# Kernel tuning notes

Measured on AMD Instinct MI355X. Metric: run time of the kernel, lower is better.

The kernel has to match this reference:

```python
import jax, jax.numpy as jnp
import numpy as np

B, S, N_USERS, N_ITEMS, E = 32, 512, 10000, 10000, 128


def setup_inputs() -> dict:
    key = jax.random.key(0)
    ks = jax.random.split(key, 8)
    users = jax.random.randint(ks[0], (B, S), 0, N_USERS, dtype=jnp.int32)
    items = jax.random.randint(ks[1], (B, S), 0, N_ITEMS, dtype=jnp.int32)
    user_mem0 = jax.random.normal(ks[2], (B, N_USERS, E), dtype=jnp.float32)
    item_mem0 = jax.random.normal(ks[3], (B, N_ITEMS, E), dtype=jnp.float32)
    # GRUCell(2E, E): w_ih (3E, 2E), w_hh (3E, E)
    w_ih = jax.random.normal(ks[4], (3 * E, 2 * E), dtype=jnp.float32) * 0.05
    w_hh = jax.random.normal(ks[5], (3 * E, E), dtype=jnp.float32) * 0.05
    b_ih = jax.random.normal(ks[6], (3 * E,), dtype=jnp.float32) * 0.05
    b_hh = jax.random.normal(ks[7], (3 * E,), dtype=jnp.float32) * 0.05
    return {"users": users, "items": items, "user_mem0": user_mem0,
            "item_mem0": item_mem0, "w_ih": w_ih, "w_hh": w_hh,
            "b_ih": b_ih, "b_hh": b_hh}


def _gru_cell(x, h, w_ih, w_hh, b_ih, b_hh):
    # torch.nn.GRUCell semantics
    gi = x @ w_ih.T + b_ih  # (B, 3E)
    gh = h @ w_hh.T + b_hh  # (B, 3E)
    i_r, i_z, i_n = jnp.split(gi, 3, axis=-1)
    h_r, h_z, h_n = jnp.split(gh, 3, axis=-1)
    r = jax.nn.sigmoid(i_r + h_r)
    z = jax.nn.sigmoid(i_z + h_z)
    n = jnp.tanh(i_n + r * h_n)
    return (1.0 - z) * n + z * h


def reference(users, items, user_mem0, item_mem0, w_ih, w_hh, b_ih, b_hh):
    batch = jnp.arange(users.shape[0])

    def step(carry, uv):
        um, im = carry
        u, it = uv  # (B,), (B,)
        ue = um[batch, u]   # gather (B, E)
        ie = im[batch, it]  # gather (B, E)
        xu = jnp.concatenate([ue, ie], axis=-1)
        xi = jnp.concatenate([ie, ue], axis=-1)
        nu = _gru_cell(xu, ue, w_ih, w_hh, b_ih, b_hh)
        ni = _gru_cell(xi, ie, w_ih, w_hh, b_ih, b_hh)
        um = um.at[batch, u].set(nu)   # scatter write
        im = im.at[batch, it].set(ni)  # scatter write
        return (um, im), (nu, ni)

    (_, _), (u_out, i_out) = jax.lax.scan(
        step, (user_mem0, item_mem0), (users.T, items.T))
    # (S, B, E) -> (B, S, E)
    return jnp.transpose(u_out, (1, 0, 2)), jnp.transpose(i_out, (1, 0, 2))
```

## Files before the change

kernel.cpp:

```cpp
#include <hip/hip_runtime.h>

#define NB 32
#define NS 512
#define NE 128
#define NU 10000

#define WS_PREVU 0
#define WS_PREVI 16384
#define WS_CNT0  32768
#define WS_CNT1  32769
#define WS_LCNT  32770
#define WS_G0    32832
#define WS_G1    49216
#define WS_LATE  65600
#define WS_WBF   81984

typedef __attribute__((ext_vector_type(8))) short bf16x8;
typedef __attribute__((ext_vector_type(4))) float f32x4;

__device__ __forceinline__ unsigned short f2bf(float f) {
    unsigned int u = __float_as_uint(f);
    u += 0x7fff + ((u >> 16) & 1);
    return (unsigned short)(u >> 16);
}

__global__ __launch_bounds__(512) void prep1_kernel(
    const int* __restrict__ users, const int* __restrict__ items,
    const float* __restrict__ w_ih, const float* __restrict__ w_hh, int* ws)
{
    const int blk = blockIdx.x, tid = threadIdx.x;
    if (blk >= 64) {
        const int base = (blk - 64) * 4096 + tid * 8;
        const int r = base >> 7, k = base & 127;
        const float* src;
        if (r < 384)      src = w_ih + (size_t)r * 256 + k;
        else if (r < 768) src = w_ih + (size_t)(r - 384) * 256 + 128 + k;
        else              src = w_hh + (size_t)(r - 768) * 128 + k;
        unsigned short* wbf = (unsigned short*)(ws + WS_WBF);
#pragma unroll
        for (int j = 0; j < 8; ++j) wbf[base + j] = f2bf(src[j]);
        return;
    }
    const int b = blk >> 1, which = blk & 1;
    if (blk == 0 && tid < 2) ws[WS_CNT0 + tid] = 0;
    __shared__ int s[NS];
    s[tid] = (which ? items : users)[b * NS + tid];
    __syncthreads();
    const int mid = s[tid];
    int p = -1;
    for (int u = tid - 1; u >= 0 && p < 0; u -= 8) {
        int vals[8];
#pragma unroll
        for (int j = 0; j < 8; ++j) {
            const int uu = u - j;
            vals[j] = (uu >= 0) ? s[uu] : -1;
        }
#pragma unroll
        for (int j = 0; j < 8; ++j)
            if (p < 0 && vals[j] == mid) p = u - j;
    }
    ws[(which ? WS_PREVI : WS_PREVU) + b * NS + tid] = p;
}

__global__ __launch_bounds__(512) void prep2_kernel(int* ws)
{
    const int b = blockIdx.x, tid = threadIdx.x;
    __shared__ short s_pU[NS], s_pI[NS];
    __shared__ unsigned char s_r[NS];
    __shared__ int c0, c1, base0, base1, s_chg;
    const int pU = ws[WS_PREVU + (b << 9) + tid];
    const int pI = ws[WS_PREVI + (b << 9) + tid];
    s_pU[tid] = (short)pU;
    s_pI[tid] = (short)pI;
    s_r[tid] = (pU < 0 && pI < 0) ? 0 : 255;
    if (tid == 0) { c0 = 0; c1 = 0; }
    __syncthreads();
    for (int pass = 0; pass < 16; ++pass) {
        if (tid == 0) s_chg = 0;
        __syncthreads();
        if (s_r[tid] == 255) {
            const int ru = pU < 0 ? -1 : (int)s_r[pU];
            const int ri = pI < 0 ? -1 : (int)s_r[pI];
            if (ru != 255 && ri != 255) {
                int rr = 1 + (ru > ri ? ru : ri);
                if (rr > 2) rr = 2;
                s_r[tid] = (unsigned char)rr;
                s_chg = 1;
            }
        }
        __syncthreads();
        if (!s_chg) break;
    }
    const int r = s_r[tid];
    int slot = -1;
    if (r == 0)      slot = atomicAdd(&c0, 1);
    else if (r == 1) slot = atomicAdd(&c1, 1);
    __syncthreads();
    if (tid == 0) {
        base0 = atomicAdd(&ws[WS_CNT0], c0);
        base1 = atomicAdd(&ws[WS_CNT1], c1);
    }
    __syncthreads();
    const int node = (b << 9) + tid;
    if (r == 0)      ws[WS_G0 + base0 + slot] = node;
    else if (r == 1) ws[WS_G1 + base1 + slot] = node;
    if (tid == 0) {
        int n = 0;
        for (int t = 0; t < NS; ++t)
            if (s_r[t] >= 2) { ws[WS_LATE + (b << 9) + n] = t; ++n; }
        ws[WS_LCNT + b] = n;
    }
}

__global__ __launch_bounds__(512, 1) void round_gemm(
    const int* __restrict__ users, const int* __restrict__ items,
    const float* __restrict__ umem0, const float* __restrict__ imem0,
    const float* __restrict__ b_ih, const float* __restrict__ b_hh,
    const int* __restrict__ ws, float* uout, float* iout,
    int cnt_off, int list_off)
{
    const int count = ws[cnt_off];
    const int nch = (count + 7) >> 3;
    if ((int)blockIdx.x >= nch) return;
    const int tid = threadIdx.x;
    const int lane = tid & 63, wave = tid >> 6;
    const int col = lane & 15, kgrp = lane >> 4;

    __shared__ __align__(16) float yl[16 * 1156];
    __shared__ __align__(16) float xf[16 * 132];
    __shared__ __align__(16) unsigned short xb[16 * 136];
    __shared__ float b6[768];
    __shared__ unsigned long long srcs[16];
    __shared__ unsigned long long hdst[16];

    for (int i = tid; i < 768; i += 512)
        b6[i] = i < 384 ? b_ih[i] : b_hh[i - 384];

    const unsigned short* wbf = (const unsigned short*)(ws + WS_WBF);
    bf16x8 wfrag[9][4];
#pragma unroll
    for (int m9 = 0; m9 < 9; ++m9) {
        const int row = wave * 144 + m9 * 16 + col;
#pragma unroll
        for (int kt = 0; kt < 4; ++kt)
            wfrag[m9][kt] = *(const bf16x8*)&wbf[row * 128 + kt * 32 + kgrp * 8];
    }

    const int* glist = ws + list_off;
    const int* prevU = ws + WS_PREVU;
    const int* prevI = ws + WS_PREVI;

    for (int ch = blockIdx.x; ch < nch; ch += gridDim.x) {
        if (tid < 16) {
            const int j = ch * 8 + (tid >> 1);
            unsigned long long sp = 0, hd = 0;
            if (j < count) {
                const int node = glist[j];
                const int bb = node >> 9;
                const int cell = tid & 1;
                const int p = cell ? prevI[node] : prevU[node];
                const float* s;
                if (p < 0) {
                    const int ix = cell ? items[node] : users[node];
                    s = (cell ? imem0 : umem0) + ((size_t)bb * NU + ix) * NE;
                } else {
                    s = (cell ? iout : uout) + ((size_t)((bb << 9) + p)) * NE;
                }
                sp = (unsigned long long)s;
                hd = (unsigned long long)((cell ? iout : uout) + (size_t)node * NE);
            }
            srcs[tid] = sp; hdst[tid] = hd;
        }
        __syncthreads();
        {
            const int c = tid >> 5, e4 = (tid & 31) * 4;
            const float* s = (const float*)srcs[c];
            if (s) {
                const float4 v = *(const float4*)(s + e4);
                *(float4*)&xf[c * 132 + e4] = v;
                ushort4 w4;
                w4.x = f2bf(v.x); w4.y = f2bf(v.y);
                w4.z = f2bf(v.z); w4.w = f2bf(v.w);
                *(ushort4*)&xb[c * 136 + e4] = w4;
            }
        }
        __syncthreads();
        {
            bf16x8 bfrag[4];
#pragma unroll
            for (int kt = 0; kt < 4; ++kt)
                bfrag[kt] = *(const bf16x8*)&xb[col * 136 + kt * 32 + kgrp * 8];
            f32x4 acc[9];
#pragma unroll
            for (int m9 = 0; m9 < 9; ++m9) acc[m9] = (f32x4){0.f, 0.f, 0.f, 0.f};
#pragma unroll
            for (int kt = 0; kt < 4; ++kt)
#pragma unroll
                for (int m9 = 0; m9 < 9; ++m9)
                    acc[m9] = __builtin_amdgcn_mfma_f32_16x16x32_bf16(
                        wfrag[m9][kt], bfrag[kt], acc[m9], 0, 0, 0);
#pragma unroll
            for (int m9 = 0; m9 < 9; ++m9)
                *(f32x4*)&yl[col * 1156 + wave * 144 + m9 * 16 + kgrp * 4] = acc[m9];
        }
        __syncthreads();
#pragma unroll
        for (int it = 0; it < 4; ++it) {
            const int idx = tid + it * 512;
            const int c = idx >> 7, e = idx & 127;
            float* hb = (float*)hdst[c];
            if (hb) {
                const float* ys = &yl[c * 1156];
                const float* yo = &yl[(c ^ 1) * 1156];
                const float gir = ys[e]        + yo[384 + e] + b6[e];
                const float giz = ys[128 + e]  + yo[512 + e] + b6[128 + e];
                const float gin = ys[256 + e]  + yo[640 + e] + b6[256 + e];
                const float ghr = ys[768 + e]  + b6[384 + e];
                const float ghz = ys[896 + e]  + b6[512 + e];
                const float ghn = ys[1024 + e] + b6[640 + e];
                const float rr = 1.f / (1.f + __expf(-(gir + ghr)));
                const float z  = 1.f / (1.f + __expf(-(giz + ghz)));
                const float pre = gin + rr * ghn;
                const float n = 2.f / (1.f + __expf(-2.f * pre)) - 1.f;
                hb[e] = (1.f - z) * n + z * xf[c * 132 + e];
            }
        }
        __syncthreads();
    }
}

__global__ __launch_bounds__(512, 1) void cleanup_kernel(
    const int* __restrict__ users, const int* __restrict__ items,
    const float* __restrict__ umem0, const float* __restrict__ imem0,
    const float* __restrict__ b_ih, const float* __restrict__ b_hh,
    const int* __restrict__ ws, float* uout, float* iout)
{
    const int b = blockIdx.x;
    const int n = ws[WS_LCNT + b];
    if (n == 0) return;
    const int tid = threadIdx.x;
    const int lane = tid & 63, wave = tid >> 6;
    const int col = lane & 15, kgrp = lane >> 4;

    __shared__ __align__(16) float yl[2][1156];
    __shared__ __align__(16) float xf[2][132];
    __shared__ __align__(16) unsigned short xb[2][136];
    __shared__ float b6[768];
    __shared__ const float* srcs[2];

    for (int i = tid; i < 768; i += 512)
        b6[i] = i < 384 ? b_ih[i] : b_hh[i - 384];

    const unsigned short* wbf = (const unsigned short*)(ws + WS_WBF);
    bf16x8 wfrag[9][4];
#pragma unroll
    for (int m9 = 0; m9 < 9; ++m9) {
        const int row = wave * 144 + m9 * 16 + col;
#pragma unroll
        for (int kt = 0; kt < 4; ++kt)
            wfrag[m9][kt] = *(const bf16x8*)&wbf[row * 128 + kt * 32 + kgrp * 8];
    }

    const int* prevU = ws + WS_PREVU;
    const int* prevI = ws + WS_PREVI;

    for (int k = 0; k < n; ++k) {
        const int t = ws[WS_LATE + (b << 9) + k];
        const int node = (b << 9) + t;
        if (tid < 2) {
            const int cell = tid;
            const int p = cell ? prevI[node] : prevU[node];
            const float* sp;
            if (p < 0) {
                const int ix = cell ? items[node] : users[node];
                sp = (cell ? imem0 : umem0) + ((size_t)b * NU + ix) * NE;
            } else {
                sp = (cell ? iout : uout) + ((size_t)((b << 9) + p)) * NE;
            }
            srcs[cell] = sp;
        }
        __syncthreads();
        if (tid < 64) {
            const int c = tid >> 5, e4 = (tid & 31) * 4;
            const float4 v = *(const float4*)(srcs[c] + e4);
            *(float4*)&xf[c][e4] = v;
            ushort4 w4;
            w4.x = f2bf(v.x); w4.y = f2bf(v.y);
            w4.z = f2bf(v.z); w4.w = f2bf(v.w);
            *(ushort4*)&xb[c][e4] = w4;
        }
        __syncthreads();
        {
            const int bc = col & 1;
            bf16x8 bfrag[4];
#pragma unroll
            for (int kt = 0; kt < 4; ++kt)
                bfrag[kt] = *(const bf16x8*)&xb[bc][kt * 32 + kgrp * 8];
            f32x4 acc[9];
#pragma unroll
            for (int m9 = 0; m9 < 9; ++m9) acc[m9] = (f32x4){0.f, 0.f, 0.f, 0.f};
#pragma unroll
            for (int kt = 0; kt < 4; ++kt)
#pragma unroll
                for (int m9 = 0; m9 < 9; ++m9)
                    acc[m9] = __builtin_amdgcn_mfma_f32_16x16x32_bf16(
                        wfrag[m9][kt], bfrag[kt], acc[m9], 0, 0, 0);
            if (col < 2) {
#pragma unroll
                for (int m9 = 0; m9 < 9; ++m9)
                    *(f32x4*)&yl[col][wave * 144 + m9 * 16 + kgrp * 4] = acc[m9];
            }
        }
        __syncthreads();
        if (tid < 256) {
            const int c = tid >> 7, e = tid & 127;
            const float* ys = yl[c];
            const float* yo = yl[c ^ 1];
            const float gir = ys[e]        + yo[384 + e] + b6[e];
            const float giz = ys[128 + e]  + yo[512 + e] + b6[128 + e];
            const float gin = ys[256 + e]  + yo[640 + e] + b6[256 + e];
            const float ghr = ys[768 + e]  + b6[384 + e];
            const float ghz = ys[896 + e]  + b6[512 + e];
            const float ghn = ys[1024 + e] + b6[640 + e];
            const float rr = 1.f / (1.f + __expf(-(gir + ghr)));
            const float z  = 1.f / (1.f + __expf(-(giz + ghz)));
            const float pre = gin + rr * ghn;
            const float nn = 2.f / (1.f + __expf(-2.f * pre) ) - 1.f;
            (c ? iout : uout)[(size_t)node * NE + e] =
                (1.f - z) * nn + z * xf[c][e];
        }
        __threadfence();
        __syncthreads();
    }
}

extern "C" void kernel_launch(void* const* d_in, const int* in_sizes, int n_in,
                              void* d_out, int out_size, void* d_ws, size_t ws_size,
                              hipStream_t stream) {
    const int*   users = (const int*)d_in[0];
    const int*   items = (const int*)d_in[1];
    const float* umem0 = (const float*)d_in[2];
    const float* imem0 = (const float*)d_in[3];
    const float* w_ih  = (const float*)d_in[4];
    const float* w_hh  = (const float*)d_in[5];
    const float* b_ih  = (const float*)d_in[6];
    const float* b_hh  = (const float*)d_in[7];

    float* uout = (float*)d_out;
    float* iout = uout + (size_t)NB * NS * NE;
    int* ws = (int*)d_ws;

    prep1_kernel<<<100, 512, 0, stream>>>(users, items, w_ih, w_hh, ws);
    prep2_kernel<<<NB, 512, 0, stream>>>(ws);
    round_gemm<<<256, 512, 0, stream>>>(users, items, umem0, imem0,
                                        b_ih, b_hh, ws, uout, iout,
                                        WS_CNT0, WS_G0);
    round_gemm<<<256, 512, 0, stream>>>(users, items, umem0, imem0,
                                        b_ih, b_hh, ws, uout, iout,
                                        WS_CNT1, WS_G1);
    cleanup_kernel<<<NB, 512, 0, stream>>>(users, items, umem0, imem0,
                                           b_ih, b_hh, ws, uout, iout);
}
```

Measured before the change: 122.5 us.

## Fuse prep kernels, add third dependency round, prefetch per-batch chunk gathers

Merges the two prep kernels into one per-batch kernel that finds previous occurrences and assigns dependency levels, now capping at level 3 so a third batched GEMM round runs before the serial cleanup. Round lists become per-batch, without global atomics, and each block handles up to 8 chunks of one batch. It gathers all chunk inputs up front into registers to hide memory latency. Lighter barriers replace __syncthreads. This shrinks the serial tail work and removes one launch, at the cost of an extra round launch and more register pressure.

```diff
diff --git a/kernel.cpp b/kernel.cpp
--- a/kernel.cpp
+++ b/kernel.cpp
@@ -7,13 +7,11 @@
 
 #define WS_PREVU 0
 #define WS_PREVI 16384
-#define WS_CNT0  32768
-#define WS_CNT1  32769
-#define WS_LCNT  32770
-#define WS_G0    32832
-#define WS_G1    49216
-#define WS_LATE  65600
-#define WS_WBF   81984
+#define WS_RCNT  32768
+#define WS_LCNT  32864
+#define WS_GL    32896
+#define WS_LATE  82048
+#define WS_WBF   98432
 
 typedef __attribute__((ext_vector_type(8))) short bf16x8;
 typedef __attribute__((ext_vector_type(4))) float f32x4;
@@ -24,13 +22,19 @@
     return (unsigned short)(u >> 16);
 }
 
-__global__ __launch_bounds__(512) void prep1_kernel(
+#define BARRIER() do { \
+    asm volatile("s_waitcnt lgkmcnt(0)" ::: "memory"); \
+    __builtin_amdgcn_s_barrier(); \
+    __builtin_amdgcn_sched_barrier(0); \
+} while (0)
+
+__global__ __launch_bounds__(512) void prep_kernel(
     const int* __restrict__ users, const int* __restrict__ items,
     const float* __restrict__ w_ih, const float* __restrict__ w_hh, int* ws)
 {
     const int blk = blockIdx.x, tid = threadIdx.x;
-    if (blk >= 64) {
-        const int base = (blk - 64) * 4096 + tid * 8;
+    if (blk >= 32) {
+        const int base = (blk - 32) * 4096 + tid * 8;
         const int r = base >> 7, k = base & 127;
         const float* src;
         if (r < 384)      src = w_ih + (size_t)r * 256 + k;
@@ -41,49 +45,51 @@
         for (int j = 0; j < 8; ++j) wbf[base + j] = f2bf(src[j]);
         return;
     }
-    const int b = blk >> 1, which = blk & 1;
-    if (blk == 0 && tid < 2) ws[WS_CNT0 + tid] = 0;
-    __shared__ int s[NS];
-    s[tid] = (which ? items : users)[b * NS + tid];
+    const int b = blk;
+    __shared__ int s_u[NS], s_i[NS];
+    __shared__ unsigned char s_r[NS];
+    __shared__ int cnt[3], s_chg;
+    s_u[tid] = users[b * NS + tid];
+    s_i[tid] = items[b * NS + tid];
+    if (tid < 3) cnt[tid] = 0;
     __syncthreads();
-    const int mid = s[tid];
-    int p = -1;
-    for (int u = tid - 1; u >= 0 && p < 0; u -= 8) {
+    const int mu = s_u[tid], mi = s_i[tid];
+    int pu = -1, pi = -1;
+    for (int u = tid - 1; u >= 0 && pu < 0; u -= 8) {
         int vals[8];
 #pragma unroll
         for (int j = 0; j < 8; ++j) {
             const int uu = u - j;
-            vals[j] = (uu >= 0) ? s[uu] : -1;
+            vals[j] = (uu >= 0) ? s_u[uu] : -1;
         }
 #pragma unroll
         for (int j = 0; j < 8; ++j)
-            if (p < 0 && vals[j] == mid) p = u - j;
-    }
-    ws[(which ? WS_PREVI : WS_PREVU) + b * NS + tid] = p;
-}
-
-__global__ __launch_bounds__(512) void prep2_kernel(int* ws)
-{
-    const int b = blockIdx.x, tid = threadIdx.x;
-    __shared__ short s_pU[NS], s_pI[NS];
-    __shared__ unsigned char s_r[NS];
-    __shared__ int c0, c1, base0, base1, s_chg;
-    const int pU = ws[WS_PREVU + (b << 9) + tid];
-    const int pI = ws[WS_PREVI + (b << 9) + tid];
-    s_pU[tid] = (short)pU;
-    s_pI[tid] = (short)pI;
-    s_r[tid] = (pU < 0 && pI < 0) ? 0 : 255;
-    if (tid == 0) { c0 = 0; c1 = 0; }
+            if (pu < 0 && vals[j] == mu) pu = u - j;
+    }
+    for (int u = tid - 1; u >= 0 && pi < 0; u -= 8) {
+        int vals[8];
+#pragma unroll
+        for (int j = 0; j < 8; ++j) {
+            const int uu = u - j;
+            vals[j] = (uu >= 0) ? s_i[uu] : -1;
+        }
+#pragma unroll
+        for (int j = 0; j < 8; ++j)
+            if (pi < 0 && vals[j] == mi) pi = u - j;
+    }
+    ws[WS_PREVU + (b << 9) + tid] = pu;
+    ws[WS_PREVI + (b << 9) + tid] = pi;
+    s_r[tid] = (pu < 0 && pi < 0) ? 0 : 255;
     __syncthreads();
     for (int pass = 0; pass < 16; ++pass) {
         if (tid == 0) s_chg = 0;
         __syncthreads();
         if (s_r[tid] == 255) {
-            const int ru = pU < 0 ? -1 : (int)s_r[pU];
-            const int ri = pI < 0 ? -1 : (int)s_r[pI];
+            const int ru = pu < 0 ? -1 : (int)s_r[pu];
+            const int ri = pi < 0 ? -1 : (int)s_r[pi];
             if (ru != 255 && ri != 255) {
                 int rr = 1 + (ru > ri ? ru : ri);
-                if (rr > 2) rr = 2;
+                if (rr > 3) rr = 3;
                 s_r[tid] = (unsigned char)rr;
                 s_chg = 1;
             }
@@ -92,22 +98,16 @@
         if (!s_chg) break;
     }
     const int r = s_r[tid];
-    int slot = -1;
-    if (r == 0)      slot = atomicAdd(&c0, 1);
-    else if (r == 1) slot = atomicAdd(&c1, 1);
+    if (r < 3) {
+        const int slot = atomicAdd(&cnt[r], 1);
+        ws[WS_GL + (r * 32 + b) * 512 + slot] = tid;
+    }
     __syncthreads();
-    if (tid == 0) {
-        base0 = atomicAdd(&ws[WS_CNT0], c0);
-        base1 = atomicAdd(&ws[WS_CNT1], c1);
-    }
-    __syncthreads();
-    const int node = (b << 9) + tid;
-    if (r == 0)      ws[WS_G0 + base0 + slot] = node;
-    else if (r == 1) ws[WS_G1 + base1 + slot] = node;
+    if (tid < 3) ws[WS_RCNT + tid * 32 + b] = cnt[tid];
     if (tid == 0) {
         int n = 0;
         for (int t = 0; t < NS; ++t)
-            if (s_r[t] >= 2) { ws[WS_LATE + (b << 9) + n] = t; ++n; }
+            if (s_r[t] >= 3) { ws[WS_LATE + (b << 9) + n] = t; ++n; }
         ws[WS_LCNT + b] = n;
     }
 }
@@ -116,12 +116,12 @@
     const int* __restrict__ users, const int* __restrict__ items,
     const float* __restrict__ umem0, const float* __restrict__ imem0,
     const float* __restrict__ b_ih, const float* __restrict__ b_hh,
-    const int* __restrict__ ws, float* uout, float* iout,
-    int cnt_off, int list_off)
+    const int* __restrict__ ws, float* uout, float* iout, int r)
 {
-    const int count = ws[cnt_off];
-    const int nch = (count + 7) >> 3;
-    if ((int)blockIdx.x >= nch) return;
+    const int b = blockIdx.x & 31, sblk = blockIdx.x >> 5;
+    const int cnt = ws[WS_RCNT + r * 32 + b];
+    const int nch = (cnt + 7) >> 3;
+    if (sblk >= nch) return;
     const int tid = threadIdx.x;
     const int lane = tid & 63, wave = tid >> 6;
     const int col = lane & 15, kgrp = lane >> 4;
@@ -130,8 +130,8 @@
     __shared__ __align__(16) float xf[16 * 132];
     __shared__ __align__(16) unsigned short xb[16 * 136];
     __shared__ float b6[768];
-    __shared__ unsigned long long srcs[16];
-    __shared__ unsigned long long hdst[16];
+    __shared__ unsigned long long srcs[8][16];
+    __shared__ unsigned long long hdst[8][16];
 
     for (int i = tid; i < 768; i += 512)
         b6[i] = i < 384 ? b_ih[i] : b_hh[i - 384];
@@ -146,45 +146,57 @@
             wfrag[m9][kt] = *(const bf16x8*)&wbf[row * 128 + kt * 32 + kgrp * 8];
     }
 
-    const int* glist = ws + list_off;
-    const int* prevU = ws + WS_PREVU;
-    const int* prevI = ws + WS_PREVI;
-
-    for (int ch = blockIdx.x; ch < nch; ch += gridDim.x) {
-        if (tid < 16) {
-            const int j = ch * 8 + (tid >> 1);
-            unsigned long long sp = 0, hd = 0;
-            if (j < count) {
-                const int node = glist[j];
-                const int bb = node >> 9;
-                const int cell = tid & 1;
-                const int p = cell ? prevI[node] : prevU[node];
+    const int* glist = ws + WS_GL + (r * 32 + b) * 512;
+    const int* prevU = ws + WS_PREVU + (b << 9);
+    const int* prevI = ws + WS_PREVI + (b << 9);
+
+    if (tid < 128) {
+        const int k = tid >> 4, idx = tid & 15;
+        const int lc = sblk + k * 8;
+        unsigned long long sp = 0, hd = 0;
+        if (lc < nch) {
+            const int j = lc * 8 + (idx >> 1);
+            if (j < cnt) {
+                const int t = glist[j];
+                const int node = (b << 9) + t;
+                const int cell = idx & 1;
+                const int p = cell ? prevI[t] : prevU[t];
                 const float* s;
                 if (p < 0) {
                     const int ix = cell ? items[node] : users[node];
-                    s = (cell ? imem0 : umem0) + ((size_t)bb * NU + ix) * NE;
+                    s = (cell ? imem0 : umem0) + ((size_t)b * NU + ix) * NE;
                 } else {
-                    s = (cell ? iout : uout) + ((size_t)((bb << 9) + p)) * NE;
+                    s = (cell ? iout : uout) + ((size_t)((b << 9) + p)) * NE;
                 }
                 sp = (unsigned long long)s;
                 hd = (unsigned long long)((cell ? iout : uout) + (size_t)node * NE);
             }
-            srcs[tid] = sp; hdst[tid] = hd;
-        }
-        __syncthreads();
-        {
-            const int c = tid >> 5, e4 = (tid & 31) * 4;
-            const float* s = (const float*)srcs[c];
-            if (s) {
-                const float4 v = *(const float4*)(s + e4);
-                *(float4*)&xf[c * 132 + e4] = v;
-                ushort4 w4;
-                w4.x = f2bf(v.x); w4.y = f2bf(v.y);
-                w4.z = f2bf(v.z); w4.w = f2bf(v.w);
-                *(ushort4*)&xb[c * 136 + e4] = w4;
-            }
-        }
-        __syncthreads();
+        }
+        srcs[k][idx] = sp; hdst[k][idx] = hd;
+    }
+    BARRIER();
+
+    const int gc = tid >> 5, ge4 = (tid & 31) * 4;
+    float4 v[8];
+#pragma unroll
+    for (int k = 0; k < 8; ++k) {
+        const float* s = (const float*)srcs[k][gc];
+        v[k] = (float4){0.f, 0.f, 0.f, 0.f};
+        if (s) v[k] = *(const float4*)(s + ge4);
+    }
+
+#pragma unroll
+    for (int k = 0; k < 8; ++k) {
+        const int lc = sblk + k * 8;
+        if (lc >= nch) break;
+        if (srcs[k][gc]) {
+            *(float4*)&xf[gc * 132 + ge4] = v[k];
+            ushort4 w4;
+            w4.x = f2bf(v[k].x); w4.y = f2bf(v[k].y);
+            w4.z = f2bf(v[k].z); w4.w = f2bf(v[k].w);
+            *(ushort4*)&xb[gc * 136 + ge4] = w4;
+        }
+        BARRIER();
         {
             bf16x8 bfrag[4];
 #pragma unroll
@@ -203,12 +215,12 @@
             for (int m9 = 0; m9 < 9; ++m9)
                 *(f32x4*)&yl[col * 1156 + wave * 144 + m9 * 16 + kgrp * 4] = acc[m9];
         }
-        __syncthreads();
+        BARRIER();
 #pragma unroll
         for (int it = 0; it < 4; ++it) {
             const int idx = tid + it * 512;
             const int c = idx >> 7, e = idx & 127;
-            float* hb = (float*)hdst[c];
+            float* hb = (float*)hdst[k][c];
             if (hb) {
                 const float* ys = &yl[c * 1156];
                 const float* yo = &yl[(c ^ 1) * 1156];
@@ -225,7 +237,7 @@
                 hb[e] = (1.f - z) * n + z * xf[c * 132 + e];
             }
         }
-        __syncthreads();
+        BARRIER();
     }
 }
 
@@ -261,15 +273,15 @@
             wfrag[m9][kt] = *(const bf16x8*)&wbf[row * 128 + kt * 32 + kgrp * 8];
     }
 
-    const int* prevU = ws + WS_PREVU;
-    const int* prevI = ws + WS_PREVI;
+    const int* prevU = ws + WS_PREVU + (b << 9);
+    const int* prevI = ws + WS_PREVI + (b << 9);
 
     for (int k = 0; k < n; ++k) {
         const int t = ws[WS_LATE + (b << 9) + k];
         const int node = (b << 9) + t;
         if (tid < 2) {
             const int cell = tid;
-            const int p = cell ? prevI[node] : prevU[node];
+            const int p = cell ? prevI[t] : prevU[t];
             const float* sp;
             if (p < 0) {
                 const int ix = cell ? items[node] : users[node];
@@ -282,11 +294,11 @@
         __syncthreads();
         if (tid < 64) {
             const int c = tid >> 5, e4 = (tid & 31) * 4;
-            const float4 v = *(const float4*)(srcs[c] + e4);
-            *(float4*)&xf[c][e4] = v;
+            const float4 vv = *(const float4*)(srcs[c] + e4);
+            *(float4*)&xf[c][e4] = vv;
             ushort4 w4;
-            w4.x = f2bf(v.x); w4.y = f2bf(v.y);
-            w4.z = f2bf(v.z); w4.w = f2bf(v.w);
+            w4.x = f2bf(vv.x); w4.y = f2bf(vv.y);
+            w4.z = f2bf(vv.z); w4.w = f2bf(vv.w);
             *(ushort4*)&xb[c][e4] = w4;
         }
         __syncthreads();
@@ -325,7 +337,7 @@
             const float rr = 1.f / (1.f + __expf(-(gir + ghr)));
             const float z  = 1.f / (1.f + __expf(-(giz + ghz)));
             const float pre = gin + rr * ghn;
-            const float nn = 2.f / (1.f + __expf(-2.f * pre) ) - 1.f;
+            const float nn = 2.f / (1.f + __expf(-2.f * pre)) - 1.f;
             (c ? iout : uout)[(size_t)node * NE + e] =
                 (1.f - z) * nn + z * xf[c][e];
         }
@@ -350,14 +362,13 @@
     float* iout = uout + (size_t)NB * NS * NE;
     int* ws = (int*)d_ws;
 
-    prep1_kernel<<<100, 512, 0, stream>>>(users, items, w_ih, w_hh, ws);
-    prep2_kernel<<<NB, 512, 0, stream>>>(ws);
+    prep_kernel<<<68, 512, 0, stream>>>(users, items, w_ih, w_hh, ws);
     round_gemm<<<256, 512, 0, stream>>>(users, items, umem0, imem0,
-                                        b_ih, b_hh, ws, uout, iout,
-                                        WS_CNT0, WS_G0);
+                                        b_ih, b_hh, ws, uout, iout, 0);
     round_gemm<<<256, 512, 0, stream>>>(users, items, umem0, imem0,
-                                        b_ih, b_hh, ws, uout, iout,
-                                        WS_CNT1, WS_G1);
+                                        b_ih, b_hh, ws, uout, iout, 1);
+    round_gemm<<<256, 512, 0, stream>>>(users, items, umem0, imem0,
+                                        b_ih, b_hh, ws, uout, iout, 2);
     cleanup_kernel<<<NB, 512, 0, stream>>>(users, items, umem0, imem0,
                                            b_ih, b_hh, ws, uout, iout);
 }
```

After: 135.4 us. 10.5% more time.
